# Kernel tuning notes

Hardware: AMD Instinct MI355X
Metric: run time of the kernel (lower is better)

## Reference

```python
import jax, jax.numpy as jnp
import numpy as np

B, T, I, H = 64, 2048, 256, 256


def setup_inputs() -> dict:
    key = jax.random.key(0)
    ks = jax.random.split(key, 6)
    s = 1.0 / np.sqrt(H)
    x = jax.random.normal(ks[0], (B, T, I), dtype=jnp.float32)
    att_weights = jax.random.uniform(ks[1], (B, T), dtype=jnp.float32)
    lengths = jax.random.randint(ks[2], (B,), 1, T + 1, dtype=jnp.int32)
    W_ih = jax.random.uniform(ks[3], (3 * H, I), minval=-s, maxval=s, dtype=jnp.float32)
    W_hh = jax.random.uniform(ks[4], (3 * H, H), minval=-s, maxval=s, dtype=jnp.float32)
    b_ih = jax.random.uniform(ks[5], (3 * H,), minval=-s, maxval=s, dtype=jnp.float32)
    b_hh = jax.random.uniform(jax.random.fold_in(key, 7), (3 * H,), minval=-s, maxval=s, dtype=jnp.float32)
    return {"x": x, "att_weights": att_weights, "lengths": lengths,
            "W_ih": W_ih, "W_hh": W_hh, "b_ih": b_ih, "b_hh": b_hh}


def reference(x, att_weights, lengths, W_ih, W_hh, b_ih, b_hh):
    # x: [B, T, I]; att_weights: [B, T]; lengths: [B]
    Bv, Tv, _ = x.shape
    Hv = W_hh.shape[1]
    # Padded equivalent of the packed-sequence loop: update h only while t < length.
    mask = jnp.arange(Tv)[None, :] < lengths[:, None]  # [B, T]

    def step(h, inp):
        xt, wt, mt = inp  # [B, I], [B], [B]
        gi = xt @ W_ih.T + b_ih  # [B, 3H]
        gh = h @ W_hh.T + b_hh   # [B, 3H]
        i_r, i_z, i_n = jnp.split(gi, 3, axis=-1)
        h_r, h_z, h_n = jnp.split(gh, 3, axis=-1)
        r = jax.nn.sigmoid(i_r + h_r)
        z = jax.nn.sigmoid(i_z + h_z)
        n = jnp.tanh(i_n + r * h_n)
        h_new = (1.0 - z) * n + z * h  # GRUCell output
        w = wt[:, None]
        h_gated = w * h_new + (1.0 - w) * h  # attention gating
        h = jnp.where(mt[:, None], h_gated, h)
        return h, None

    h0 = jnp.zeros((Bv, Hv), dtype=x.dtype)
    xs = (jnp.swapaxes(x, 0, 1), att_weights.T, mask.T)  # time-major
    hT, _ = jax.lax.scan(step, h0, xs)
    return hT  # [B, H]
```

## Files before the change

### kernel.cpp

```cpp
#include <hip/hip_runtime.h>
#include <stdint.h>

#define B_ 64
#define T_ 2048
#define I_ 256
#define H_ 256
#define G3 768
#define NPROD 192
#define CH 16
#define NTILE_N 6

typedef _Float16 half2v __attribute__((ext_vector_type(2)));
typedef _Float16 half8v __attribute__((ext_vector_type(8)));

#if __has_builtin(__builtin_amdgcn_fdot2)
#define FDOT2(a, b, c) __builtin_amdgcn_fdot2((a), (b), (c), false)
#else
#define FDOT2(a, b, c) fmaf((float)(a)[1], (float)(b)[1], fmaf((float)(a)[0], (float)(b)[0], (c)))
#endif

__global__ void zero_flags(int* __restrict__ done, int n)
{
  int i = threadIdx.x + blockIdx.x * blockDim.x;
  if (i < n) __hip_atomic_store(&done[i], 0, __ATOMIC_RELAXED, __HIP_MEMORY_SCOPE_AGENT);
}

__global__ __launch_bounds__(512) __attribute__((amdgpu_waves_per_eu(2, 2)))
void fused(const float* __restrict__ x, const float* __restrict__ att,
           const int* __restrict__ lengths, const float* __restrict__ Wih,
           const float* __restrict__ Whh, const float* __restrict__ bih,
           const float* __restrict__ bhh, float* __restrict__ gi,
           int* __restrict__ done, float* __restrict__ hws,
           float* __restrict__ out, int t0, int t1)
{
  __shared__ __align__(16) float smem[32 * 68 + 32 * 132];
  const int tid = threadIdx.x;
  const int Tc = t1 - t0;

  if (blockIdx.x >= B_) {
    const int pid = blockIdx.x - B_;
    float* As = smem;
    float* Bs = smem + 32 * 68;
    const int ty = tid >> 5, tx = tid & 31;
    const int lr = tid >> 3;
    const int lk = (tid & 7) << 2;
    const int NT = Tc * NTILE_N;
    for (int i = pid; i < NT; i += NPROD) {
      const int rel = i / NTILE_N;
      const int tt  = t0 + rel;
      const int n0  = (i % NTILE_N) << 7;
      float acc[4][4] = {};
      for (int kc = 0; kc < I_; kc += 32) {
        float4 a0 = *(const float4*)(x + ((size_t)lr * T_ + tt) * I_ + kc + lk);
        float4 b0 = *(const float4*)(Wih + (size_t)(n0 + lr) * I_ + kc + lk);
        float4 b1 = *(const float4*)(Wih + (size_t)(n0 + lr + 64) * I_ + kc + lk);
        __syncthreads();
        As[(lk + 0) * 68 + lr] = a0.x; As[(lk + 1) * 68 + lr] = a0.y;
        As[(lk + 2) * 68 + lr] = a0.z; As[(lk + 3) * 68 + lr] = a0.w;
        Bs[(lk + 0) * 132 + lr] = b0.x; Bs[(lk + 1) * 132 + lr] = b0.y;
        Bs[(lk + 2) * 132 + lr] = b0.z; Bs[(lk + 3) * 132 + lr] = b0.w;
        Bs[(lk + 0) * 132 + lr + 64] = b1.x; Bs[(lk + 1) * 132 + lr + 64] = b1.y;
        Bs[(lk + 2) * 132 + lr + 64] = b1.z; Bs[(lk + 3) * 132 + lr + 64] = b1.w;
        __syncthreads();
        #pragma unroll
        for (int kk = 0; kk < 32; ++kk) {
          float4 av = *(const float4*)(&As[kk * 68 + (ty << 2)]);
          float4 bv = *(const float4*)(&Bs[kk * 132 + (tx << 2)]);
          float av_[4] = {av.x, av.y, av.z, av.w};
          float bv_[4] = {bv.x, bv.y, bv.z, bv.w};
          #pragma unroll
          for (int u = 0; u < 4; ++u)
            #pragma unroll
            for (int v = 0; v < 4; ++v)
              acc[u][v] = fmaf(av_[u], bv_[v], acc[u][v]);
        }
      }
      const int colb = n0 + (tx << 2);
      float4 bi = *(const float4*)(bih + colb);
      float4 bh = *(const float4*)(bhh + colb);
      float4 badd;
      badd.x = bi.x + (colb + 0 < 512 ? bh.x : 0.f);
      badd.y = bi.y + (colb + 1 < 512 ? bh.y : 0.f);
      badd.z = bi.z + (colb + 2 < 512 ? bh.z : 0.f);
      badd.w = bi.w + (colb + 3 < 512 ? bh.w : 0.f);
      float* gout = gi + (size_t)rel * B_ * G3;
      #pragma unroll
      for (int r = 0; r < 4; ++r) {
        const int bb = (ty << 2) + r;
        float4 o;
        o.x = acc[r][0] + badd.x; o.y = acc[r][1] + badd.y;
        o.z = acc[r][2] + badd.z; o.w = acc[r][3] + badd.w;
        *(float4*)(gout + (size_t)bb * G3 + colb) = o;
      }
      __syncthreads();
      if (tid == 0) {
        __threadfence();
        __hip_atomic_fetch_add(&done[rel >> 4], 1, __ATOMIC_RELEASE, __HIP_MEMORY_SCOPE_AGENT);
      }
    }
    return;
  }

  const int b  = blockIdx.x;
  const int j  = tid >> 1;
  const int s  = tid & 1;
  const int k0 = s << 7;
  _Float16* hbuf = (_Float16*)smem;

  half2v w[192];
  #pragma unroll
  for (int g = 0; g < 3; ++g) {
    const float* row = Whh + (size_t)(g * 256 + j) * H_ + k0;
    #pragma unroll
    for (int q = 0; q < 32; ++q) {
      float4 v = *(const float4*)(row + (q << 2));
      half2v a, c;
      a[0] = (_Float16)v.x; a[1] = (_Float16)v.y;
      c[0] = (_Float16)v.z; c[1] = (_Float16)v.w;
      w[g * 64 + 2 * q]     = a;
      w[g * 64 + 2 * q + 1] = c;
    }
  }

  float bhn = 0.f, h_reg = 0.f;
  if (s == 0) {
    bhn = bhh[512 + j];
    h_reg = (t0 > 0) ? hws[b * H_ + j] : 0.f;
  }
  if (tid < 256) {
    float v = (t0 > 0) ? hws[b * H_ + tid] : 0.f;
    hbuf[(tid >> 7) * 136 + (tid & 127)] = (_Float16)v;
  }
  int len = lengths[b]; if (len > t1) len = t1;
  const int nch = (Tc + CH - 1) / CH;
  int wm = -1;
  __syncthreads();

#define GATE(NEED) do {                                                               \
    int need_ = (NEED); if (need_ > nch - 1) need_ = nch - 1;                         \
    if (need_ > wm) {                                                                 \
      if (tid == 0) {                                                                 \
        for (int c_ = wm + 1; c_ <= need_; ++c_) {                                    \
          int exp_ = ((Tc - c_ * CH) < CH ? (Tc - c_ * CH) : CH) * NTILE_N;           \
          while (__hip_atomic_load(&done[c_], __ATOMIC_RELAXED,                       \
                                   __HIP_MEMORY_SCOPE_AGENT) < exp_)                  \
            __builtin_amdgcn_s_sleep(2);                                              \
        }                                                                             \
      }                                                                               \
      __syncthreads();                                                                \
      __threadfence();             \
      wm = need_;                                                                     \
    }                                                                                 \
  } while (0)

#define STEP(GR, GZ, GN, WAT, TT, RELOAD_OK) do {                                     \
    float accr = 0.f, accz = 0.f, accn = 0.f;                                         \
    const _Float16* hb = hbuf + p * 272 + s * 136;                                    \
    _Pragma("unroll")                                                                 \
    for (int q = 0; q < 16; ++q) {                                                    \
      half8v hv = *(const half8v*)(hb + (q << 3));                                    \
      half2v h0_ = __builtin_shufflevector(hv, hv, 0, 1);                             \
      half2v h1_ = __builtin_shufflevector(hv, hv, 2, 3);                             \
      half2v h2_ = __builtin_shufflevector(hv, hv, 4, 5);                             \
      half2v h3_ = __builtin_shufflevector(hv, hv, 6, 7);                             \
      const int qq = q << 2;                                                          \
      accr = FDOT2(w[qq + 0], h0_, accr);                                             \
      accr = FDOT2(w[qq + 1], h1_, accr);                                             \
      accr = FDOT2(w[qq + 2], h2_, accr);                                             \
      accr = FDOT2(w[qq + 3], h3_, accr);                                             \
      accz = FDOT2(w[64 + qq + 0], h0_, accz);                                        \
      accz = FDOT2(w[64 + qq + 1], h1_, accz);                                        \
      accz = FDOT2(w[64 + qq + 2], h2_, accz);                                        \
      accz = FDOT2(w[64 + qq + 3], h3_, accz);                                        \
      accn = FDOT2(w[128 + qq + 0], h0_, accn);                                       \
      accn = FDOT2(w[128 + qq + 1], h1_, accn);                                       \
      accn = FDOT2(w[128 + qq + 2], h2_, accn);                                       \
      accn = FDOT2(w[128 + qq + 3], h3_, accn);                                       \
    }                                                                                 \
    accr += __shfl_xor(accr, 1);                                                      \
    accz += __shfl_xor(accz, 1);                                                      \
    accn += __shfl_xor(accn, 1);                                                      \
    if (s == 0) {                                                                     \
      float r_ = 1.f / (1.f + __expf(-(accr + GR)));                                  \
      float z_ = 1.f / (1.f + __expf(-(accz + GZ)));                                  \
      float e2_ = __expf(2.f * (GN + r_ * (accn + bhn)));                             \
      float nn_ = 1.f - 2.f / (e2_ + 1.f);                                            \
      float hnew_ = (1.f - z_) * nn_ + z_ * h_reg;                                    \
      h_reg = (WAT) * hnew_ + (1.f - (WAT)) * h_reg;                                  \
      hbuf[(p ^ 1) * 272 + (j >> 7) * 136 + (j & 127)] = (_Float16)h_reg;             \
      if (RELOAD_OK) {                                                                \
        const float* gb_ = gi + ((size_t)((TT) + 2 - t0) * B_ + b) * G3;              \
        GR = gb_[j]; GZ = gb_[256 + j]; GN = gb_[512 + j];                            \
        WAT = att[(size_t)b * T_ + (TT) + 2];                                         \
      }                                                                               \
    }                                                                                 \
    __syncthreads();                                                                  \
    p ^= 1;                                                                           \
  } while (0)

  GATE(0);
  float e_gr = 0.f, e_gz = 0.f, e_gn = 0.f, e_wat = 0.f;
  float o_gr = 0.f, o_gz = 0.f, o_gn = 0.f, o_wat = 0.f;
  if (s == 0 && t0 < len) {
    const float* gb = gi + (size_t)b * G3;
    e_gr = gb[j]; e_gz = gb[256 + j]; e_gn = gb[512 + j];
    e_wat = att[(size_t)b * T_ + t0];
  }
  if (s == 0 && t0 + 1 < len) {
    const float* gb = gi + ((size_t)B_ + b) * G3;
    o_gr = gb[j]; o_gz = gb[256 + j]; o_gn = gb[512 + j];
    o_wat = att[(size_t)b * T_ + t0 + 1];
  }

  int p = 0;
  int t = t0;
  for (; t + 1 < len; t += 2) {
    GATE((t + 3 - t0) >> 4);
    STEP(e_gr, e_gz, e_gn, e_wat, t,     (t + 2 < len));
    STEP(o_gr, o_gz, o_gn, o_wat, t + 1, (t + 3 < len));
  }
  if (t < len) {
    STEP(e_gr, e_gz, e_gn, e_wat, t, false);
  }

  if (s == 0) {
    hws[b * H_ + j] = h_reg;
    if (t1 == T_) out[b * H_ + j] = h_reg;
  }
#undef STEP
#undef GATE
}

extern "C" void kernel_launch(void* const* d_in, const int* in_sizes, int n_in,
                              void* d_out, int out_size, void* d_ws, size_t ws_size,
                              hipStream_t stream)
{
  const float* x       = (const float*)d_in[0];
  const float* att     = (const float*)d_in[1];
  const int*   lengths = (const int*)d_in[2];
  const float* Wih     = (const float*)d_in[3];
  const float* Whh     = (const float*)d_in[4];
  const float* bih     = (const float*)d_in[5];
  const float* bhh     = (const float*)d_in[6];
  float* out = (float*)d_out;

  int*   done = (int*)d_ws;
  float* hws  = (float*)((char*)d_ws + 4096);
  float* gi   = (float*)((char*)d_ws + 4096 + 65536);
  const size_t used0 = 4096 + 65536;
  const size_t per_t = (size_t)B_ * G3 * sizeof(float);
  size_t avail = ws_size > used0 ? ws_size - used0 : 0;
  int Tc = (int)(avail / per_t);
  if (Tc > T_) Tc = T_;
  if (Tc < 1) Tc = 1;

  for (int t0 = 0; t0 < T_; t0 += Tc) {
    int t1 = t0 + Tc; if (t1 > T_) t1 = T_;
    int nch = (t1 - t0 + CH - 1) / CH;
    zero_flags<<<dim3((nch + 127) / 128), 128, 0, stream>>>(done, nch);
    fused<<<dim3(B_ + NPROD), 512, 0, stream>>>(x, att, lengths, Wih, Whh, bih, bhh,
                                                gi, done, hws, out, t0, t1);
  }
}
```

Baseline: 3.738 ms.

## Throttle gi producers to a bounded lead over recurrent consumer progress

Each recurrent block now publishes its current timestep to a per-batch progress flag. Producer blocks take the minimum across all 64 flags and wait until their tile lies within a fixed window (LEADW) ahead of it. The aim is to keep freshly produced gi rows hot in cache and to reduce producer memory pressure on the latency-bound recurrent loop. The two-step unrolled STEP macro is replaced by a single-step loop that prefetches the next step's gi and attention weight before the dot products. The spin-waiting adds polling traffic, and the next-step gi load now sits closer to the critical path.

Result: slower. 3.852 ms (+3.1%).

```diff
diff --git a/kernel.cpp b/kernel.cpp
--- a/kernel.cpp
+++ b/kernel.cpp
@@ -9,6 +9,7 @@
 #define NPROD 192
 #define CH 16
 #define NTILE_N 6
+#define LEADW 192
 
 typedef _Float16 half2v __attribute__((ext_vector_type(2)));
 typedef _Float16 half8v __attribute__((ext_vector_type(8)));
@@ -36,6 +37,7 @@
   __shared__ __align__(16) float smem[32 * 68 + 32 * 132];
   const int tid = threadIdx.x;
   const int Tc = t1 - t0;
+  int* const prog = done + 128;
 
   if (blockIdx.x >= B_) {
     const int pid = blockIdx.x - B_;
@@ -49,6 +51,23 @@
       const int rel = i / NTILE_N;
       const int tt  = t0 + rel;
       const int n0  = (i % NTILE_N) << 7;
+
+      if (tid < 64) {
+        for (;;) {
+          int pv = __hip_atomic_load(&prog[tid], __ATOMIC_RELAXED, __HIP_MEMORY_SCOPE_AGENT);
+          int m = pv;
+          m = min(m, __shfl_xor(m, 32));
+          m = min(m, __shfl_xor(m, 16));
+          m = min(m, __shfl_xor(m, 8));
+          m = min(m, __shfl_xor(m, 4));
+          m = min(m, __shfl_xor(m, 2));
+          m = min(m, __shfl_xor(m, 1));
+          if (rel < m + LEADW) break;
+          __builtin_amdgcn_s_sleep(8);
+        }
+      }
+      __syncthreads();
+
       float acc[4][4] = {};
       for (int kc = 0; kc < I_; kc += 32) {
         float4 a0 = *(const float4*)(x + ((size_t)lr * T_ + tt) * I_ + kc + lk);
@@ -136,10 +155,12 @@
   int wm = -1;
   __syncthreads();
 
-#define GATE(NEED) do {                                                               \
+#define GATE(NEED, TCUR) do {                                                         \
     int need_ = (NEED); if (need_ > nch - 1) need_ = nch - 1;                         \
     if (need_ > wm) {                                                                 \
       if (tid == 0) {                                                                 \
+        __hip_atomic_store(&prog[b], (TCUR) - t0, __ATOMIC_RELAXED,                   \
+                           __HIP_MEMORY_SCOPE_AGENT);                                 \
         for (int c_ = wm + 1; c_ <= need_; ++c_) {                                    \
           int exp_ = ((Tc - c_ * CH) < CH ? (Tc - c_ * CH) : CH) * NTILE_N;           \
           while (__hip_atomic_load(&done[c_], __ATOMIC_RELAXED,                       \
@@ -148,86 +169,77 @@
         }                                                                             \
       }                                                                               \
       __syncthreads();                                                                \
-      __threadfence();             \
+      __threadfence();       \
       wm = need_;                                                                     \
     }                                                                                 \
   } while (0)
 
-#define STEP(GR, GZ, GN, WAT, TT, RELOAD_OK) do {                                     \
-    float accr = 0.f, accz = 0.f, accn = 0.f;                                         \
-    const _Float16* hb = hbuf + p * 272 + s * 136;                                    \
-    _Pragma("unroll")                                                                 \
-    for (int q = 0; q < 16; ++q) {                                                    \
-      half8v hv = *(const half8v*)(hb + (q << 3));                                    \
-      half2v h0_ = __builtin_shufflevector(hv, hv, 0, 1);                             \
-      half2v h1_ = __builtin_shufflevector(hv, hv, 2, 3);                             \
-      half2v h2_ = __builtin_shufflevector(hv, hv, 4, 5);                             \
-      half2v h3_ = __builtin_shufflevector(hv, hv, 6, 7);                             \
-      const int qq = q << 2;                                                          \
-      accr = FDOT2(w[qq + 0], h0_, accr);                                             \
-      accr = FDOT2(w[qq + 1], h1_, accr);                                             \
-      accr = FDOT2(w[qq + 2], h2_, accr);                                             \
-      accr = FDOT2(w[qq + 3], h3_, accr);                                             \
-      accz = FDOT2(w[64 + qq + 0], h0_, accz);                                        \
-      accz = FDOT2(w[64 + qq + 1], h1_, accz);                                        \
-      accz = FDOT2(w[64 + qq + 2], h2_, accz);                                        \
-      accz = FDOT2(w[64 + qq + 3], h3_, accz);                                        \
-      accn = FDOT2(w[128 + qq + 0], h0_, accn);                                       \
-      accn = FDOT2(w[128 + qq + 1], h1_, accn);                                       \
-      accn = FDOT2(w[128 + qq + 2], h2_, accn);                                       \
-      accn = FDOT2(w[128 + qq + 3], h3_, accn);                                       \
-    }                                                                                 \
-    accr += __shfl_xor(accr, 1);                                                      \
-    accz += __shfl_xor(accz, 1);                                                      \
-    accn += __shfl_xor(accn, 1);                                                      \
-    if (s == 0) {                                                                     \
-      float r_ = 1.f / (1.f + __expf(-(accr + GR)));                                  \
-      float z_ = 1.f / (1.f + __expf(-(accz + GZ)));                                  \
-      float e2_ = __expf(2.f * (GN + r_ * (accn + bhn)));                             \
-      float nn_ = 1.f - 2.f / (e2_ + 1.f);                                            \
-      float hnew_ = (1.f - z_) * nn_ + z_ * h_reg;                                    \
-      h_reg = (WAT) * hnew_ + (1.f - (WAT)) * h_reg;                                  \
-      hbuf[(p ^ 1) * 272 + (j >> 7) * 136 + (j & 127)] = (_Float16)h_reg;             \
-      if (RELOAD_OK) {                                                                \
-        const float* gb_ = gi + ((size_t)((TT) + 2 - t0) * B_ + b) * G3;              \
-        GR = gb_[j]; GZ = gb_[256 + j]; GN = gb_[512 + j];                            \
-        WAT = att[(size_t)b * T_ + (TT) + 2];                                         \
-      }                                                                               \
-    }                                                                                 \
-    __syncthreads();                                                                  \
-    p ^= 1;                                                                           \
-  } while (0)
-
-  GATE(0);
-  float e_gr = 0.f, e_gz = 0.f, e_gn = 0.f, e_wat = 0.f;
-  float o_gr = 0.f, o_gz = 0.f, o_gn = 0.f, o_wat = 0.f;
+  GATE(0, t0);
+  float c_gr = 0.f, c_gz = 0.f, c_gn = 0.f, c_wat = 0.f;
   if (s == 0 && t0 < len) {
     const float* gb = gi + (size_t)b * G3;
-    e_gr = gb[j]; e_gz = gb[256 + j]; e_gn = gb[512 + j];
-    e_wat = att[(size_t)b * T_ + t0];
-  }
-  if (s == 0 && t0 + 1 < len) {
-    const float* gb = gi + ((size_t)B_ + b) * G3;
-    o_gr = gb[j]; o_gz = gb[256 + j]; o_gn = gb[512 + j];
-    o_wat = att[(size_t)b * T_ + t0 + 1];
+    c_gr = gb[j]; c_gz = gb[256 + j]; c_gn = gb[512 + j];
+    c_wat = att[(size_t)b * T_ + t0];
   }
 
   int p = 0;
-  int t = t0;
-  for (; t + 1 < len; t += 2) {
-    GATE((t + 3 - t0) >> 4);
-    STEP(e_gr, e_gz, e_gn, e_wat, t,     (t + 2 < len));
-    STEP(o_gr, o_gz, o_gn, o_wat, t + 1, (t + 3 < len));
-  }
-  if (t < len) {
-    STEP(e_gr, e_gz, e_gn, e_wat, t, false);
-  }
-
+  for (int t = t0; t < len; ++t) {
+    GATE((t + 1 - t0) >> 4, t);
+    float n_gr = 0.f, n_gz = 0.f, n_gn = 0.f, n_wat = 0.f;
+    if (s == 0 && t + 1 < len) {
+      const float* gb = gi + ((size_t)(t + 1 - t0) * B_ + b) * G3;
+      n_gr = gb[j]; n_gz = gb[256 + j]; n_gn = gb[512 + j];
+      n_wat = att[(size_t)b * T_ + t + 1];
+    }
+
+    float accr = 0.f, accz = 0.f, accn = 0.f;
+    const _Float16* hb = hbuf + p * 272 + s * 136;
+    #pragma unroll
+    for (int q = 0; q < 16; ++q) {
+      half8v hv = *(const half8v*)(hb + (q << 3));
+      half2v h0 = __builtin_shufflevector(hv, hv, 0, 1);
+      half2v h1 = __builtin_shufflevector(hv, hv, 2, 3);
+      half2v h2 = __builtin_shufflevector(hv, hv, 4, 5);
+      half2v h3 = __builtin_shufflevector(hv, hv, 6, 7);
+      const int qq = q << 2;
+      accr = FDOT2(w[qq + 0], h0, accr);
+      accr = FDOT2(w[qq + 1], h1, accr);
+      accr = FDOT2(w[qq + 2], h2, accr);
+      accr = FDOT2(w[qq + 3], h3, accr);
+      accz = FDOT2(w[64 + qq + 0], h0, accz);
+      accz = FDOT2(w[64 + qq + 1], h1, accz);
+      accz = FDOT2(w[64 + qq + 2], h2, accz);
+      accz = FDOT2(w[64 + qq + 3], h3, accz);
+      accn = FDOT2(w[128 + qq + 0], h0, accn);
+      accn = FDOT2(w[128 + qq + 1], h1, accn);
+      accn = FDOT2(w[128 + qq + 2], h2, accn);
+      accn = FDOT2(w[128 + qq + 3], h3, accn);
+    }
+    accr += __shfl_xor(accr, 1);
+    accz += __shfl_xor(accz, 1);
+    accn += __shfl_xor(accn, 1);
+
+    if (s == 0) {
+      float r = 1.f / (1.f + __expf(-(accr + c_gr)));
+      float z = 1.f / (1.f + __expf(-(accz + c_gz)));
+      float e2 = __expf(2.f * (c_gn + r * (accn + bhn)));
+      float nn = 1.f - 2.f / (e2 + 1.f);
+      float hnew = (1.f - z) * nn + z * h_reg;
+      h_reg = c_wat * hnew + (1.f - c_wat) * h_reg;
+      hbuf[(p ^ 1) * 272 + (j >> 7) * 136 + (j & 127)] = (_Float16)h_reg;
+    }
+    __syncthreads();
+    p ^= 1;
+    c_gr = n_gr; c_gz = n_gz; c_gn = n_gn; c_wat = n_wat;
+  }
+
+  if (tid == 0) {
+    __hip_atomic_store(&prog[b], Tc, __ATOMIC_RELAXED, __HIP_MEMORY_SCOPE_AGENT);
+  }
   if (s == 0) {
     hws[b * H_ + j] = h_reg;
     if (t1 == T_) out[b * H_ + j] = h_reg;
   }
-#undef STEP
 #undef GATE
 }
 
@@ -257,7 +269,9 @@
   for (int t0 = 0; t0 < T_; t0 += Tc) {
     int t1 = t0 + Tc; if (t1 > T_) t1 = T_;
     int nch = (t1 - t0 + CH - 1) / CH;
-    zero_flags<<<dim3((nch + 127) / 128), 128, 0, stream>>>(done, nch);
+    int nflags = 128 + B_;
+    (void)nch;
+    zero_flags<<<dim3((nflags + 127) / 128), 128, 0, stream>>>(done, nflags);
     fused<<<dim3(B_ + NPROD), 512, 0, stream>>>(x, att, lengths, Wih, Whh, bih, bhh,
                                                 gi, done, hws, out, t0, t1);
   }
```
